# Kernel tuning notes

Measured on AMD Instinct MI355X. Metric: run time of the kernel, lower is better.

Reference implementation:

```python
import jax, jax.numpy as jnp
import numpy as np

N, IN_DIM, OUT_DIM, HEADS = 2048, 512, 512, 8
HEAD_DIM = OUT_DIM // HEADS
NEG_SLOPE = 0.2


def setup_inputs() -> dict:
    key = jax.random.key(0)
    k1, k2, k3, k4 = jax.random.split(key, 4)
    x = jax.random.normal(k1, (N, IN_DIM), dtype=jnp.float32)
    adj = jax.random.randint(k2, (N, N), 0, 2, dtype=jnp.int32)
    W = jax.random.normal(k3, (IN_DIM, OUT_DIM), dtype=jnp.float32) * 0.02
    a = jax.random.normal(k4, (2 * HEAD_DIM,), dtype=jnp.float32) * 0.02
    return {"x": x, "adj": adj, "W": W, "a": a}


def reference(x, adj, W, a):
    # Wh: (N, H, Dh)
    Wh = (x @ W).reshape(N, HEADS, HEAD_DIM)
    # a . concat(Wh_i, Wh_j) == (Wh_i . a_src) + (Wh_j . a_dst) -- exact decomposition,
    # avoids materializing the (N, N, H, 2*Dh) concat tensor.
    a_src, a_dst = a[:HEAD_DIM], a[HEAD_DIM:]
    s_i = jnp.einsum('nhd,d->nh', Wh, a_src)  # contribution of dest node i
    s_j = jnp.einsum('nhd,d->nh', Wh, a_dst)  # contribution of source node j
    e = jax.nn.leaky_relu(s_i[:, None, :] + s_j[None, :, :], negative_slope=NEG_SLOPE)  # (N, N, H)
    mask = (adj > 0)[:, :, None]
    e = jnp.where(mask, e, jnp.float32(-jnp.inf))
    alpha = jax.nn.softmax(e, axis=1)  # softmax over source nodes j
    # out[i,h,:] = sum_j alpha[i,j,h] * Wh[j,h,:]   (dropout is identity at eval)
    out = jnp.einsum('ijh,jhd->ihd', alpha, Wh)
    return out.reshape(N, OUT_DIM)
```

## Files before the change

kernel.cpp:

```cpp
#include <hip/hip_runtime.h>
#include <hip/hip_bf16.h>

#define NN 2048
#define KD 512
#define ODIM 512
#define NHEAD 8
#define HD 64
#define NEG 0.2f

typedef float f32x4 __attribute__((ext_vector_type(4)));
typedef short bf16x8 __attribute__((ext_vector_type(8)));
typedef short bf16x4 __attribute__((ext_vector_type(4)));
typedef unsigned long long u64;
typedef unsigned int u32;

__device__ __forceinline__ short tob(float f) {
  __hip_bfloat16 h = __float2bfloat16(f);
  return *reinterpret_cast<short*>(&h);
}

__device__ __forceinline__ void gl_lds16(const void* g, void* l) {
  __builtin_amdgcn_global_load_lds(
      (const __attribute__((address_space(1))) u32*)g,
      (__attribute__((address_space(3))) u32*)l, 16, 0, 0);
}

__global__ __launch_bounds__(256) void prep(const float* __restrict__ X,
                                            const float* __restrict__ W,
                                            const int* __restrict__ adj,
                                            short* __restrict__ Xf,
                                            short* __restrict__ Bf,
                                            unsigned short* __restrict__ bits) {
  __shared__ float sbuf[16 * 516];
  const int b = blockIdx.x;
  const int t = threadIdx.x;

  if (b < 1024) {
    const int T = b * 256 + t;
    const int row = T >> 7, g = T & 127;
    const int* p = adj + (size_t)row * NN + g * 16;
    u32 m = 0;
#pragma unroll
    for (int q = 0; q < 4; ++q) {
      const int4 v = *(const int4*)&p[q * 4];
      m |= (v.x > 0 ? 1u : 0u) << (q * 4);
      m |= (v.y > 0 ? 2u : 0u) << (q * 4);
      m |= (v.z > 0 ? 4u : 0u) << (q * 4);
      m |= (v.w > 0 ? 8u : 0u) << (q * 4);
    }
    bits[T] = (unsigned short)m;
    return;
  }

  if (b < 1024 + 128) {
    const int xb = b - 1024;
#pragma unroll
    for (int q = 0; q < 8; ++q) {
      const int flat = q * 256 + t;
      const int row = flat >> 7, c4 = flat & 127;
      const float4 v = *(const float4*)&X[(size_t)(xb * 16 + row) * KD + c4 * 4];
      *(float4*)&sbuf[row * 516 + c4 * 4] = v;
    }
    __syncthreads();
#pragma unroll
    for (int c = 0; c < 4; ++c) {
      const int s = c * 256 + t;
      const int l = s & 63;
      const int col = l & 15, kg = (l >> 4) & 3;
      const int k0 = (s >> 6) * 32 + kg * 8;
      bf16x8 o;
#pragma unroll
      for (int u = 0; u < 8; ++u) o[u] = tob(sbuf[col * 516 + k0 + u]);
      *(bf16x8*)&Xf[((size_t)xb * 1024 + s) * 8] = o;
    }
    return;
  }

  const int b2 = b - 1152;
  const int kb = b2 & 7, h = b2 >> 3;
  const int k0 = kb * 64;
#pragma unroll
  for (int q = 0; q < 4; ++q) {
    const int flat = q * 256 + t;
    const int kk = flat >> 4, o4 = (flat & 15) * 4;
    const float4 v = *(const float4*)&W[(size_t)(k0 + kk) * ODIM + h * 64 + o4];
    *(float4*)&sbuf[kk * 68 + o4] = v;
  }
  __syncthreads();
#pragma unroll
  for (int c = 0; c < 2; ++c) {
    const int s = c * 256 + t;
    const int ksl = s >> 8, nt = (s >> 6) & 3, l = s & 63;
    const int col = l & 15, kg = (l >> 4) & 3;
    const int kloc = ksl * 32 + kg * 8;
    const int od = nt * 16 + col;
    bf16x8 o;
#pragma unroll
    for (int u = 0; u < 8; ++u) o[u] = tob(sbuf[(kloc + u) * 68 + od]);
    const size_t off = (((size_t)(h * 4 + nt) * 16 + kb * 2 + ksl) * 64 + l) * 8;
    *(bf16x8*)&Bf[off] = o;
  }
}

__global__ __launch_bounds__(256) void gemm_fused(
    const short* __restrict__ Xf, const short* __restrict__ Bf,
    const float* __restrict__ a, short* __restrict__ WhF,
    float2* __restrict__ esrcp, u32* __restrict__ edstp) {
  const int t = threadIdx.x;
  const int lane = t & 63, w = t >> 6;
  const int col = lane & 15, kgrp = lane >> 4;
  const int bm = blockIdx.x * 64;
  const int h = blockIdx.y;
  const int mt = blockIdx.x * 4 + w;

  const short* ax = Xf + (size_t)mt * 8192;
  const short* bx = Bf + (size_t)h * 32768;

  f32x4 acc[4] = {};

#pragma unroll
  for (int ks = 0; ks < 16; ++ks) {
    const bf16x8 af = *(const bf16x8*)&ax[(ks * 64 + lane) * 8];
#pragma unroll
    for (int nt = 0; nt < 4; ++nt) {
      const bf16x8 bf = *(const bf16x8*)&bx[((nt * 16 + ks) * 64 + lane) * 8];
      acc[nt] = __builtin_amdgcn_mfma_f32_16x16x32_bf16(af, bf, acc[nt], 0, 0, 0);
    }
  }

  float asv[4], adv[4];
#pragma unroll
  for (int nt = 0; nt < 4; ++nt) {
    asv[nt] = a[nt * 16 + col];
    adv[nt] = a[64 + nt * 16 + col];
  }
  float ps[4], pd[4];
#pragma unroll
  for (int r = 0; r < 4; ++r) {
    float s1 = 0.f, s2 = 0.f;
#pragma unroll
    for (int nt = 0; nt < 4; ++nt) {
      s1 += acc[nt][r] * asv[nt];
      s2 += acc[nt][r] * adv[nt];
    }
    ps[r] = s1;
    pd[r] = s2;
  }
#pragma unroll
  for (int off = 1; off <= 8; off <<= 1) {
#pragma unroll
    for (int r = 0; r < 4; ++r) {
      ps[r] += __shfl_xor(ps[r], off);
      pd[r] += __shfl_xor(pd[r], off);
    }
  }
  {
    const size_t tbase = ((size_t)h * 32 + blockIdx.x) * 4096;
    const int lp = ((w & 1) * 2 + (kgrp >> 1)) * 16 + col;
    const int u0 = (kgrp & 1) * 4;
    const int slot_ks = w >> 1;
#pragma unroll
    for (int nt = 0; nt < 4; ++nt) {
      bf16x4 o;
#pragma unroll
      for (int r = 0; r < 4; ++r) o[r] = tob(acc[nt][r]);
      *(bf16x4*)&WhF[tbase + (size_t)(nt * 2 + slot_ks) * 512 + lp * 8 + u0] = o;
    }
  }
  if (col == 0) {
    const int mbase = bm + w * 16 + kgrp * 4;
#pragma unroll
    for (int r = 0; r < 4; ++r) {
      const int n = mbase + r;
      esrcp[h * NN + n] = make_float2(__expf(ps[r]), __expf(NEG * ps[r]));
      const u32 lo = (u32)(unsigned short)tob(__expf(pd[r]));
      const u32 hi = (u32)(unsigned short)tob(__expf(NEG * pd[r]));
      edstp[h * NN + n] = (hi << 16) | lo;
    }
  }
}

__global__ __launch_bounds__(256) void attn_mfma(
    const short* __restrict__ WhF, const unsigned char* __restrict__ adjbits,
    const float2* __restrict__ esrcp, const u32* __restrict__ edstp,
    float* __restrict__ out) {
  extern __shared__ __align__(16) char smem[];
  const int t = threadIdx.x;
  const int lane = t & 63;
  const int jq = t >> 6;
  const int col = lane & 15, kgrp = lane >> 4;
  const int h = blockIdx.y;
  const int i0 = blockIdx.x * 32;
  char* wbase = smem + jq * 20480;
  char* dbuf = wbase;
  char* elds = wbase + 16384;
  char* albs = wbase + 18432;

  const short* tb = WhF + ((size_t)h * 32 + jq * 8) * 4096;
  const int jb = jq * 512;

  const float2 e0 = esrcp[h * NN + i0 + col];
  const float2 e1 = esrcp[h * NN + i0 + 16 + col];
  const float A0 = e0.x, C0 = e0.y, A1 = e1.x, C1 = e1.y;

  bf16x8 ones;
#pragma unroll
  for (int u = 0; u < 8; ++u) ones[u] = (short)0x3F80;

  f32x4 acc[2][4] = {};
  f32x4 accd[2] = {};

  {
#pragma unroll
    for (int d = 0; d < 2; ++d)
      gl_lds16(edstp + h * NN + jb + d * 256 + lane * 4, elds + d * 1024);
#pragma unroll
    for (int d = 0; d < 2; ++d)
      gl_lds16(adjbits + (size_t)(i0 + d * 16 + (lane >> 2)) * (NN / 8) +
                   jq * 64 + (lane & 3) * 16,
               albs + d * 1024);
#pragma unroll
    for (int s = 0; s < 8; ++s)
      gl_lds16(tb + s * 512 + lane * 8, dbuf + s * 1024);
  }

#pragma unroll
  for (int tt = 0; tt < 8; ++tt) {
    const int cur = tt & 1, nxt = cur ^ 1;

    if (tt < 7) {
      const short* g = tb + (size_t)(tt + 1) * 4096;
      char* sb = dbuf + nxt * 8192;
#pragma unroll
      for (int s = 0; s < 8; ++s)
        gl_lds16(g + s * 512 + lane * 8, sb + s * 1024);
      asm volatile("s_waitcnt vmcnt(8)" ::: "memory");
    } else {
      asm volatile("s_waitcnt vmcnt(0)" ::: "memory");
    }
    __builtin_amdgcn_sched_barrier(0);

    const u32* eu = (const u32*)elds;
    const u64 m0 = *(const u64*)(albs + col * 64 + tt * 8);
    const u64 m1 = *(const u64*)(albs + (16 + col) * 64 + tt * 8);
    bf16x8 af0[2], af1[2];
#pragma unroll
    for (int ks = 0; ks < 2; ++ks) {
      const uint4 q0 = *(const uint4*)&eu[tt * 64 + ks * 32 + kgrp * 8];
      const uint4 q1 = *(const uint4*)&eu[tt * 64 + ks * 32 + kgrp * 8 + 4];
      const u32 mb0 = (u32)(m0 >> ((ks * 4 + kgrp) * 8)) & 0xffu;
      const u32 mb1 = (u32)(m1 >> ((ks * 4 + kgrp) * 8)) & 0xffu;
      const u32 uw[8] = {q0.x, q0.y, q0.z, q0.w, q1.x, q1.y, q1.z, q1.w};
#pragma unroll
      for (int u2 = 0; u2 < 8; ++u2) {
        const float B = __uint_as_float(uw[u2] << 16);
        const float D = __uint_as_float(uw[u2] & 0xffff0000u);
        float p0 = fmaxf(A0 * B, C0 * D);
        float p1 = fmaxf(A1 * B, C1 * D);
        p0 = ((mb0 >> u2) & 1u) ? p0 : 0.f;
        p1 = ((mb1 >> u2) & 1u) ? p1 : 0.f;
        af0[ks][u2] = tob(p0);
        af1[ks][u2] = tob(p1);
      }
    }

    const short* sb = (const short*)(dbuf + cur * 8192);
    __builtin_amdgcn_s_setprio(1);
    accd[0] = __builtin_amdgcn_mfma_f32_16x16x32_bf16(af0[0], ones, accd[0], 0, 0, 0);
    accd[0] = __builtin_amdgcn_mfma_f32_16x16x32_bf16(af0[1], ones, accd[0], 0, 0, 0);
    accd[1] = __builtin_amdgcn_mfma_f32_16x16x32_bf16(af1[0], ones, accd[1], 0, 0, 0);
    accd[1] = __builtin_amdgcn_mfma_f32_16x16x32_bf16(af1[1], ones, accd[1], 0, 0, 0);
#pragma unroll
    for (int nt = 0; nt < 4; ++nt) {
      const bf16x8 b0 = *(const bf16x8*)&sb[(nt * 2 + 0) * 512 + lane * 8];
      const bf16x8 b1 = *(const bf16x8*)&sb[(nt * 2 + 1) * 512 + lane * 8];
      acc[0][nt] = __builtin_amdgcn_mfma_f32_16x16x32_bf16(af0[0], b0, acc[0][nt], 0, 0, 0);
      acc[1][nt] = __builtin_amdgcn_mfma_f32_16x16x32_bf16(af1[0], b0, acc[1][nt], 0, 0, 0);
      acc[0][nt] = __builtin_amdgcn_mfma_f32_16x16x32_bf16(af0[1], b1, acc[0][nt], 0, 0, 0);
      acc[1][nt] = __builtin_amdgcn_mfma_f32_16x16x32_bf16(af1[1], b1, acc[1][nt], 0, 0, 0);
    }
    __builtin_amdgcn_s_setprio(0);
  }

  __syncthreads();
  float* red = (float*)smem;
  float* rw = red + (size_t)jq * 32 * 66;
#pragma unroll
  for (int mt = 0; mt < 2; ++mt) {
#pragma unroll
    for (int nt = 0; nt < 4; ++nt)
#pragma unroll
      for (int r = 0; r < 4; ++r)
        rw[(mt * 16 + kgrp * 4 + r) * 66 + nt * 16 + col] = acc[mt][nt][r];
    if (col == 0) {
#pragma unroll
      for (int r = 0; r < 4; ++r)
        rw[(mt * 16 + kgrp * 4 + r) * 66 + 64] = accd[mt][r];
    }
  }
  __syncthreads();

  const int d = t & 63, rl = t >> 6;
#pragma unroll
  for (int rr = 0; rr < 8; ++rr) {
    const int row = rr * 4 + rl;
    float v = 0.f, dd = 0.f;
#pragma unroll
    for (int q = 0; q < 4; ++q) {
      v += red[((size_t)q * 32 + row) * 66 + d];
      dd += red[((size_t)q * 32 + row) * 66 + 64];
    }
    out[(size_t)(i0 + row) * ODIM + h * HD + d] = v / dd;
  }
}

extern "C" void kernel_launch(void* const* d_in, const int* in_sizes, int n_in,
                              void* d_out, int out_size, void* d_ws,
                              size_t ws_size, hipStream_t stream) {
  const float* x = (const float*)d_in[0];
  const int* adj = (const int*)d_in[1];
  const float* W = (const float*)d_in[2];
  const float* a = (const float*)d_in[3];
  float* out = (float*)d_out;

  char* ws = (char*)d_ws;
  short* WhF = (short*)ws;
  short* Xf = (short*)(ws + (2 << 20));
  short* Bf = (short*)(ws + (4 << 20));
  unsigned short* bits =
      (unsigned short*)(ws + (4 << 20) + (512 << 10));
  float2* esrcp = (float2*)(ws + (5 << 20));
  u32* edstp = (u32*)(ws + (5 << 20) + (128 << 10));

  prep<<<1216, 256, 0, stream>>>(x, W, adj, Xf, Bf, bits);
  gemm_fused<<<dim3(32, 8), 256, 0, stream>>>(Xf, Bf, a, WhF, esrcp, edstp);
  attn_mfma<<<dim3(64, 8), 256, 81920, stream>>>(
      WhF, (const unsigned char*)bits, esrcp, edstp, out);
}
```

Before: 36.57 us.

## Split attention waves by row half and GEMM by K half for more parallelism

```diff
diff --git a/kernel.cpp b/kernel.cpp
--- a/kernel.cpp
+++ b/kernel.cpp
@@ -11,6 +11,7 @@
 typedef float f32x4 __attribute__((ext_vector_type(4)));
 typedef short bf16x8 __attribute__((ext_vector_type(8)));
 typedef short bf16x4 __attribute__((ext_vector_type(4)));
+typedef unsigned int u32x4 __attribute__((ext_vector_type(4)));
 typedef unsigned long long u64;
 typedef unsigned int u32;
 
@@ -24,6 +25,15 @@
       (const __attribute__((address_space(1))) u32*)g,
       (__attribute__((address_space(3))) u32*)l, 16, 0, 0);
 }
+
+__device__ __forceinline__ u32 to_lds(const void* p) {
+  return (u32)(size_t)(const __attribute__((address_space(3))) char*)p;
+}
+
+#define DSR(dst, addr, OFFLIT)                      \
+  asm volatile("ds_read_b128 %0, %1 offset:" OFFLIT \
+               : "=v"(dst)                          \
+               : "v"(addr))
 
 __global__ __launch_bounds__(256) void prep(const float* __restrict__ X,
                                             const float* __restrict__ W,
@@ -106,122 +116,151 @@
     const short* __restrict__ Xf, const short* __restrict__ Bf,
     const float* __restrict__ a, short* __restrict__ WhF,
     float2* __restrict__ esrcp, u32* __restrict__ edstp) {
+  __shared__ float pbuf[4 * 4 * 64 * 4];
   const int t = threadIdx.x;
   const int lane = t & 63, w = t >> 6;
   const int col = lane & 15, kgrp = lane >> 4;
-  const int bm = blockIdx.x * 64;
+  const int bx = blockIdx.x;
   const int h = blockIdx.y;
-  const int mt = blockIdx.x * 4 + w;
-
-  const short* ax = Xf + (size_t)mt * 8192;
-  const short* bx = Bf + (size_t)h * 32768;
-
-  f32x4 acc[4] = {};
-
-#pragma unroll
-  for (int ks = 0; ks < 16; ++ks) {
-    const bf16x8 af = *(const bf16x8*)&ax[(ks * 64 + lane) * 8];
+  const int i0 = bx * 32;
+
+  {
+    const int mtg = bx * 2 + (w & 1);
+    const int kh = w >> 1;
+    const short* ax = Xf + (size_t)mtg * 8192;
+    const short* bxp = Bf + (size_t)h * 32768;
+
+    f32x4 acc1[4] = {};
+#pragma unroll
+    for (int k2 = 0; k2 < 8; ++k2) {
+      const int ks = kh * 8 + k2;
+      const bf16x8 af = *(const bf16x8*)&ax[(ks * 64 + lane) * 8];
+#pragma unroll
+      for (int nt = 0; nt < 4; ++nt) {
+        const bf16x8 bf = *(const bf16x8*)&bxp[((nt * 16 + ks) * 64 + lane) * 8];
+        acc1[nt] = __builtin_amdgcn_mfma_f32_16x16x32_bf16(af, bf, acc1[nt], 0, 0, 0);
+      }
+    }
+#pragma unroll
+    for (int nt = 0; nt < 4; ++nt)
+      *(f32x4*)&pbuf[((w * 4 + nt) * 64 + lane) * 4] = acc1[nt];
+  }
+  __syncthreads();
+
+  if (w < 2) {
+    f32x4 acc[4];
 #pragma unroll
     for (int nt = 0; nt < 4; ++nt) {
-      const bf16x8 bf = *(const bf16x8*)&bx[((nt * 16 + ks) * 64 + lane) * 8];
-      acc[nt] = __builtin_amdgcn_mfma_f32_16x16x32_bf16(af, bf, acc[nt], 0, 0, 0);
-    }
-  }
-
-  float asv[4], adv[4];
-#pragma unroll
-  for (int nt = 0; nt < 4; ++nt) {
-    asv[nt] = a[nt * 16 + col];
-    adv[nt] = a[64 + nt * 16 + col];
-  }
-  float ps[4], pd[4];
-#pragma unroll
-  for (int r = 0; r < 4; ++r) {
-    float s1 = 0.f, s2 = 0.f;
+      const f32x4 p0 = *(const f32x4*)&pbuf[((w * 4 + nt) * 64 + lane) * 4];
+      const f32x4 p1 = *(const f32x4*)&pbuf[(((w + 2) * 4 + nt) * 64 + lane) * 4];
+      acc[nt] = p0 + p1;
+    }
+    float asv[4], adv[4];
 #pragma unroll
     for (int nt = 0; nt < 4; ++nt) {
-      s1 += acc[nt][r] * asv[nt];
-      s2 += acc[nt][r] * adv[nt];
-    }
-    ps[r] = s1;
-    pd[r] = s2;
-  }
-#pragma unroll
-  for (int off = 1; off <= 8; off <<= 1) {
+      asv[nt] = a[nt * 16 + col];
+      adv[nt] = a[64 + nt * 16 + col];
+    }
+    float ps[4], pd[4];
 #pragma unroll
     for (int r = 0; r < 4; ++r) {
-      ps[r] += __shfl_xor(ps[r], off);
-      pd[r] += __shfl_xor(pd[r], off);
-    }
-  }
-  {
-    const size_t tbase = ((size_t)h * 32 + blockIdx.x) * 4096;
-    const int lp = ((w & 1) * 2 + (kgrp >> 1)) * 16 + col;
-    const int u0 = (kgrp & 1) * 4;
-    const int slot_ks = w >> 1;
-#pragma unroll
-    for (int nt = 0; nt < 4; ++nt) {
-      bf16x4 o;
-#pragma unroll
-      for (int r = 0; r < 4; ++r) o[r] = tob(acc[nt][r]);
-      *(bf16x4*)&WhF[tbase + (size_t)(nt * 2 + slot_ks) * 512 + lp * 8 + u0] = o;
-    }
-  }
-  if (col == 0) {
-    const int mbase = bm + w * 16 + kgrp * 4;
-#pragma unroll
-    for (int r = 0; r < 4; ++r) {
-      const int n = mbase + r;
-      esrcp[h * NN + n] = make_float2(__expf(ps[r]), __expf(NEG * ps[r]));
-      const u32 lo = (u32)(unsigned short)tob(__expf(pd[r]));
-      const u32 hi = (u32)(unsigned short)tob(__expf(NEG * pd[r]));
-      edstp[h * NN + n] = (hi << 16) | lo;
-    }
-  }
-}
-
-__global__ __launch_bounds__(256) void attn_mfma(
+      float s1 = 0.f, s2 = 0.f;
+#pragma unroll
+      for (int nt = 0; nt < 4; ++nt) {
+        s1 += acc[nt][r] * asv[nt];
+        s2 += acc[nt][r] * adv[nt];
+      }
+      ps[r] = s1;
+      pd[r] = s2;
+    }
+#pragma unroll
+    for (int off = 1; off <= 8; off <<= 1) {
+#pragma unroll
+      for (int r = 0; r < 4; ++r) {
+        ps[r] += __shfl_xor(ps[r], off);
+        pd[r] += __shfl_xor(pd[r], off);
+      }
+    }
+    {
+      const size_t tbase = ((size_t)h * 32 + (bx >> 1)) * 4096;
+      const int lp = (w * 2 + (kgrp >> 1)) * 16 + col;
+      const int u0 = (kgrp & 1) * 4;
+      const int slot_ks = bx & 1;
+#pragma unroll
+      for (int nt = 0; nt < 4; ++nt) {
+        bf16x4 o;
+#pragma unroll
+        for (int r = 0; r < 4; ++r) o[r] = tob(acc[nt][r]);
+        *(bf16x4*)&WhF[tbase + (size_t)(nt * 2 + slot_ks) * 512 + lp * 8 + u0] = o;
+      }
+    }
+    if (col == 0) {
+      const int mbase = i0 + w * 16 + kgrp * 4;
+#pragma unroll
+      for (int r = 0; r < 4; ++r) {
+        const int n = mbase + r;
+        esrcp[h * NN + n] = make_float2(__expf(ps[r]), __expf(NEG * ps[r]));
+        const u32 lo = (u32)(unsigned short)tob(__expf(pd[r]));
+        const u32 hi = (u32)(unsigned short)tob(__expf(NEG * pd[r]));
+        edstp[h * NN + n] = (hi << 16) | lo;
+      }
+    }
+  }
+}
+
+__global__ __launch_bounds__(512, 4) void attn_mfma(
     const short* __restrict__ WhF, const unsigned char* __restrict__ adjbits,
     const float2* __restrict__ esrcp, const u32* __restrict__ edstp,
     float* __restrict__ out) {
   extern __shared__ __align__(16) char smem[];
   const int t = threadIdx.x;
   const int lane = t & 63;
-  const int jq = t >> 6;
+  const int wid = t >> 6;
+  const int jq = wid & 3;
+  const int mh = wid >> 2;
   const int col = lane & 15, kgrp = lane >> 4;
   const int h = blockIdx.y;
   const int i0 = blockIdx.x * 32;
-  char* wbase = smem + jq * 20480;
-  char* dbuf = wbase;
-  char* elds = wbase + 16384;
-  char* albs = wbase + 18432;
+  const int irow = i0 + mh * 16;
+
+  char* qbase = smem + jq * 18432;
+  char* dbuf = qbase;
+  char* elds = qbase + 16384;
 
   const short* tb = WhF + ((size_t)h * 32 + jq * 8) * 4096;
   const int jb = jq * 512;
 
-  const float2 e0 = esrcp[h * NN + i0 + col];
-  const float2 e1 = esrcp[h * NN + i0 + 16 + col];
-  const float A0 = e0.x, C0 = e0.y, A1 = e1.x, C1 = e1.y;
+  const float2 e0 = esrcp[h * NN + irow + col];
+  const float A0 = e0.x, C0 = e0.y;
+
+  u64 aw[8];
+  {
+    const unsigned char* rb = adjbits + (size_t)(irow + col) * (NN / 8) + jq * 64;
+#pragma unroll
+    for (int q = 0; q < 4; ++q) {
+      const uint4 v = *(const uint4*)(rb + q * 16);
+      aw[q * 2] = (u64)v.x | ((u64)v.y << 32);
+      aw[q * 2 + 1] = (u64)v.z | ((u64)v.w << 32);
+    }
+  }
 
   bf16x8 ones;
 #pragma unroll
   for (int u = 0; u < 8; ++u) ones[u] = (short)0x3F80;
 
-  f32x4 acc[2][4] = {};
-  f32x4 accd[2] = {};
+  f32x4 acc[4] = {};
+  f32x4 accd = {};
+
+  const u32 lread = to_lds(dbuf) + (u32)lane * 16u;
+  const u32 eread = to_lds(elds) + (u32)kgrp * 32u;
 
   {
-#pragma unroll
-    for (int d = 0; d < 2; ++d)
-      gl_lds16(edstp + h * NN + jb + d * 256 + lane * 4, elds + d * 1024);
-#pragma unroll
-    for (int d = 0; d < 2; ++d)
-      gl_lds16(adjbits + (size_t)(i0 + d * 16 + (lane >> 2)) * (NN / 8) +
-                   jq * 64 + (lane & 3) * 16,
-               albs + d * 1024);
-#pragma unroll
-    for (int s = 0; s < 8; ++s)
-      gl_lds16(tb + s * 512 + lane * 8, dbuf + s * 1024);
+    gl_lds16(edstp + h * NN + jb + mh * 256 + lane * 4, elds + mh * 1024);
+#pragma unroll
+    for (int s = 0; s < 4; ++s) {
+      const int slot = mh * 4 + s;
+      gl_lds16(tb + slot * 512 + lane * 8, dbuf + slot * 1024);
+    }
   }
 
 #pragma unroll
@@ -232,83 +271,98 @@
       const short* g = tb + (size_t)(tt + 1) * 4096;
       char* sb = dbuf + nxt * 8192;
 #pragma unroll
-      for (int s = 0; s < 8; ++s)
-        gl_lds16(g + s * 512 + lane * 8, sb + s * 1024);
-      asm volatile("s_waitcnt vmcnt(8)" ::: "memory");
+      for (int s = 0; s < 4; ++s) {
+        const int slot = mh * 4 + s;
+        gl_lds16(g + slot * 512 + lane * 8, sb + slot * 1024);
+      }
+      asm volatile("s_waitcnt vmcnt(4)" ::: "memory");
     } else {
       asm volatile("s_waitcnt vmcnt(0)" ::: "memory");
     }
     __builtin_amdgcn_sched_barrier(0);
-
-    const u32* eu = (const u32*)elds;
-    const u64 m0 = *(const u64*)(albs + col * 64 + tt * 8);
-    const u64 m1 = *(const u64*)(albs + (16 + col) * 64 + tt * 8);
-    bf16x8 af0[2], af1[2];
+    __builtin_amdgcn_s_barrier();
+
+    const u32 abuf = lread + (u32)(cur * 8192);
+    bf16x8 b0, b1, b2, b3, b4, b5, b6, b7;
+    DSR(b0, abuf, "0");
+    DSR(b1, abuf, "1024");
+    DSR(b2, abuf, "2048");
+    DSR(b3, abuf, "3072");
+    DSR(b4, abuf, "4096");
+    DSR(b5, abuf, "5120");
+    DSR(b6, abuf, "6144");
+    DSR(b7, abuf, "7168");
+    u32x4 eq[4];
+    switch (tt) {
+      case 0: DSR(eq[0], eread, "0");    DSR(eq[1], eread, "16");   DSR(eq[2], eread, "128");  DSR(eq[3], eread, "144");  break;
+      case 1: DSR(eq[0], eread, "256");  DSR(eq[1], eread, "272");  DSR(eq[2], eread, "384");  DSR(eq[3], eread, "400");  break;
+      case 2: DSR(eq[0], eread, "512");  DSR(eq[1], eread, "528");  DSR(eq[2], eread, "640");  DSR(eq[3], eread, "656");  break;
+      case 3: DSR(eq[0], eread, "768");  DSR(eq[1], eread, "784");  DSR(eq[2], eread, "896");  DSR(eq[3], eread, "912");  break;
+      case 4: DSR(eq[0], eread, "1024"); DSR(eq[1], eread, "1040"); DSR(eq[2], eread, "1152"); DSR(eq[3], eread, "1168"); break;
+      case 5: DSR(eq[0], eread, "1280"); DSR(eq[1], eread, "1296"); DSR(eq[2], eread, "1408"); DSR(eq[3], eread, "1424"); break;
+      case 6: DSR(eq[0], eread, "1536"); DSR(eq[1], eread, "1552"); DSR(eq[2], eread, "1664"); DSR(eq[3], eread, "1680"); break;
+      default:DSR(eq[0], eread, "1792"); DSR(eq[1], eread, "1808"); DSR(eq[2], eread, "1920"); DSR(eq[3], eread, "1936"); break;
+    }
+    asm volatile("s_waitcnt lgkmcnt(0)" ::: "memory");
+    __builtin_amdgcn_sched_barrier(0);
+
+    bf16x8 af[2];
 #pragma unroll
     for (int ks = 0; ks < 2; ++ks) {
-      const uint4 q0 = *(const uint4*)&eu[tt * 64 + ks * 32 + kgrp * 8];
-      const uint4 q1 = *(const uint4*)&eu[tt * 64 + ks * 32 + kgrp * 8 + 4];
-      const u32 mb0 = (u32)(m0 >> ((ks * 4 + kgrp) * 8)) & 0xffu;
-      const u32 mb1 = (u32)(m1 >> ((ks * 4 + kgrp) * 8)) & 0xffu;
-      const u32 uw[8] = {q0.x, q0.y, q0.z, q0.w, q1.x, q1.y, q1.z, q1.w};
+      const u32 mb = (u32)(aw[tt] >> ((ks * 4 + kgrp) * 8)) & 0xffu;
+      const u32x4 q0 = eq[ks * 2], q1 = eq[ks * 2 + 1];
+      const u32 uw[8] = {q0[0], q0[1], q0[2], q0[3], q1[0], q1[1], q1[2], q1[3]};
 #pragma unroll
       for (int u2 = 0; u2 < 8; ++u2) {
         const float B = __uint_as_float(uw[u2] << 16);
         const float D = __uint_as_float(uw[u2] & 0xffff0000u);
-        float p0 = fmaxf(A0 * B, C0 * D);
-        float p1 = fmaxf(A1 * B, C1 * D);
-        p0 = ((mb0 >> u2) & 1u) ? p0 : 0.f;
-        p1 = ((mb1 >> u2) & 1u) ? p1 : 0.f;
-        af0[ks][u2] = tob(p0);
-        af1[ks][u2] = tob(p1);
-      }
-    }
-
-    const short* sb = (const short*)(dbuf + cur * 8192);
+        float p = fmaxf(A0 * B, C0 * D);
+        p = ((mb >> u2) & 1u) ? p : 0.f;
+        af[ks][u2] = tob(p);
+      }
+    }
+
     __builtin_amdgcn_s_setprio(1);
-    accd[0] = __builtin_amdgcn_mfma_f32_16x16x32_bf16(af0[0], ones, accd[0], 0, 0, 0);
-    accd[0] = __builtin_amdgcn_mfma_f32_16x16x32_bf16(af0[1], ones, accd[0], 0, 0, 0);
-    accd[1] = __builtin_amdgcn_mfma_f32_16x16x32_bf16(af1[0], ones, accd[1], 0, 0, 0);
-    accd[1] = __builtin_amdgcn_mfma_f32_16x16x32_bf16(af1[1], ones, accd[1], 0, 0, 0);
-#pragma unroll
-    for (int nt = 0; nt < 4; ++nt) {
-      const bf16x8 b0 = *(const bf16x8*)&sb[(nt * 2 + 0) * 512 + lane * 8];
-      const bf16x8 b1 = *(const bf16x8*)&sb[(nt * 2 + 1) * 512 + lane * 8];
-      acc[0][nt] = __builtin_amdgcn_mfma_f32_16x16x32_bf16(af0[0], b0, acc[0][nt], 0, 0, 0);
-      acc[1][nt] = __builtin_amdgcn_mfma_f32_16x16x32_bf16(af1[0], b0, acc[1][nt], 0, 0, 0);
-      acc[0][nt] = __builtin_amdgcn_mfma_f32_16x16x32_bf16(af0[1], b1, acc[0][nt], 0, 0, 0);
-      acc[1][nt] = __builtin_amdgcn_mfma_f32_16x16x32_bf16(af1[1], b1, acc[1][nt], 0, 0, 0);
-    }
+    accd = __builtin_amdgcn_mfma_f32_16x16x32_bf16(af[0], ones, accd, 0, 0, 0);
+    accd = __builtin_amdgcn_mfma_f32_16x16x32_bf16(af[1], ones, accd, 0, 0, 0);
+    acc[0] = __builtin_amdgcn_mfma_f32_16x16x32_bf16(af[0], b0, acc[0], 0, 0, 0);
+    acc[0] = __builtin_amdgcn_mfma_f32_16x16x32_bf16(af[1], b1, acc[0], 0, 0, 0);
+    acc[1] = __builtin_amdgcn_mfma_f32_16x16x32_bf16(af[0], b2, acc[1], 0, 0, 0);
+    acc[1] = __builtin_amdgcn_mfma_f32_16x16x32_bf16(af[1], b3, acc[1], 0, 0, 0);
+    acc[2] = __builtin_amdgcn_mfma_f32_16x16x32_bf16(af[0], b4, acc[2], 0, 0, 0);
+    acc[2] = __builtin_amdgcn_mfma_f32_16x16x32_bf16(af[1], b5, acc[2], 0, 0, 0);
+    acc[3] = __builtin_amdgcn_mfma_f32_16x16x32_bf16(af[0], b6, acc[3], 0, 0, 0);
+    acc[3] = __builtin_amdgcn_mfma_f32_16x16x32_bf16(af[1], b7, acc[3], 0, 0, 0);
     __builtin_amdgcn_s_setprio(0);
+
+    __builtin_amdgcn_s_barrier();
   }
 
   __syncthreads();
   float* red = (float*)smem;
-  float* rw = red + (size_t)jq * 32 * 66;
-#pragma unroll
-  for (int mt = 0; mt < 2; ++mt) {
-#pragma unroll
-    for (int nt = 0; nt < 4; ++nt)
-#pragma unroll
-      for (int r = 0; r < 4; ++r)
-        rw[(mt * 16 + kgrp * 4 + r) * 66 + nt * 16 + col] = acc[mt][nt][r];
-    if (col == 0) {
-#pragma unroll
-      for (int r = 0; r < 4; ++r)
-        rw[(mt * 16 + kgrp * 4 + r) * 66 + 64] = accd[mt][r];
-    }
+  float* rw = red + (size_t)((mh * 4 + jq) * 16) * 66;
+#pragma unroll
+  for (int nt = 0; nt < 4; ++nt)
+#pragma unroll
+    for (int r = 0; r < 4; ++r)
+      rw[(kgrp * 4 + r) * 66 + nt * 16 + col] = acc[nt][r];
+  if (col == 0) {
+#pragma unroll
+    for (int r = 0; r < 4; ++r) rw[(kgrp * 4 + r) * 66 + 64] = accd[r];
   }
   __syncthreads();
 
-  const int d = t & 63, rl = t >> 6;
-#pragma unroll
-  for (int rr = 0; rr < 8; ++rr) {
-    const int row = rr * 4 + rl;
+  const int d = t & 63, idx = t >> 6;
+#pragma unroll
+  for (int rr = 0; rr < 4; ++rr) {
+    const int row = rr * 8 + idx;
+    const int mh2 = row >> 4, r16 = row & 15;
     float v = 0.f, dd = 0.f;
 #pragma unroll
     for (int q = 0; q < 4; ++q) {
-      v += red[((size_t)q * 32 + row) * 66 + d];
-      dd += red[((size_t)q * 32 + row) * 66 + 64];
+      const float* rb = red + (size_t)((mh2 * 4 + q) * 16 + r16) * 66;
+      v += rb[d];
+      dd += rb[64];
     }
     out[(size_t)(i0 + row) * ODIM + h * HD + d] = v / dd;
   }
@@ -333,7 +387,7 @@
   u32* edstp = (u32*)(ws + (5 << 20) + (128 << 10));
 
   prep<<<1216, 256, 0, stream>>>(x, W, adj, Xf, Bf, bits);
-  gemm_fused<<<dim3(32, 8), 256, 0, stream>>>(Xf, Bf, a, WhF, esrcp, edstp);
-  attn_mfma<<<dim3(64, 8), 256, 81920, stream>>>(
+  gemm_fused<<<dim3(64, 8), 256, 0, stream>>>(Xf, Bf, a, WhF, esrcp, edstp);
+  attn_mfma<<<dim3(64, 8), 512, 73728, stream>>>(
       WhF, (const unsigned char*)bits, esrcp, edstp, out);
 }
```

New measurement: 34.86 us. 4.7% less time.
